# Kernel optimization log

Hardware: AMD Instinct MI355X
Metric: run time of the kernel (lower is better)

## Reference

```python
import jax, jax.numpy as jnp
import numpy as np
from jax import lax

EPS = 1e-5
NUM_HEADS = 8


def _safe_norm(x):
    # sqrt(max(sum x^2, EPS^2)) == max(||x||, EPS); grad-safe at 0
    return jnp.sqrt(jnp.maximum(jnp.sum(x * x, axis=-1, keepdims=True), EPS * EPS))


def _project(x):
    norm = _safe_norm(x)
    max_norm = 1.0 - EPS
    scale = jnp.where(norm >= max_norm, max_norm / (norm + EPS), jnp.ones_like(norm))
    return x * scale


def _logmap0(y):
    # logarithmic_map(0, y): lambda_0 = 2/(1+EPS)
    y = _project(y)
    n = _safe_norm(y)  # clamp(min=EPS) is built in
    lam = 2.0 / (1.0 + EPS)
    return (2.0 / lam) * jnp.arctanh(n) * (y / n)


def _expmap0(v):
    # exponential_map(0, v): lambda_0 = 2/(1+EPS)
    n = _safe_norm(v)
    lam = 2.0 / (1.0 + EPS)
    return _project(jnp.tanh(lam * n / 2.0) * (v / n))


def _mobius_add(x, y):
    x = _project(x)
    y = _project(y)
    xy = jnp.sum(x * y, axis=-1, keepdims=True)
    xn = jnp.sum(x * x, axis=-1, keepdims=True)
    yn = jnp.sum(y * y, axis=-1, keepdims=True)
    num = (1.0 + 2.0 * xy + yn) * x + (1.0 - xn) * y
    den = 1.0 + 2.0 * xy + xn * yn + EPS
    return _project(num / den)


def _hyp_linear(x, W, b):
    # HyperbolicLinear.forward: project -> logmap0 -> linear -> expmap0 -> mobius-add bias
    x = _project(x)
    xt = _logmap0(x)
    t = xt @ W.T
    r = _expmap0(t)
    r = _mobius_add(r, jnp.broadcast_to(b, r.shape))
    return r


def setup_inputs() -> dict:
    key = jax.random.key(0)
    ks = jax.random.split(key, 11)
    B, S, E = 4, 512, 512

    def xavier(k, shape):
        bound = np.sqrt(6.0 / (shape[0] + shape[1]))
        return jax.random.uniform(k, shape, jnp.float32, -bound, bound)

    return {
        "query": jax.random.normal(ks[0], (B, S, E), jnp.float32),
        "key": jax.random.normal(ks[1], (B, S, E), jnp.float32),
        "value": jax.random.normal(ks[2], (B, S, E), jnp.float32),
        "Wq": xavier(ks[3], (E, E)), "bq": 0.01 * jax.random.normal(ks[4], (E,), jnp.float32),
        "Wk": xavier(ks[5], (E, E)), "bk": 0.01 * jax.random.normal(ks[6], (E,), jnp.float32),
        "Wv": xavier(ks[7], (E, E)), "bv": 0.01 * jax.random.normal(ks[8], (E,), jnp.float32),
        "Wo": xavier(ks[9], (E, E)), "bo": 0.01 * jax.random.normal(ks[10], (E,), jnp.float32),
    }


def reference(query, key, value, Wq, bq, Wk, bk, Wv, bv, Wo, bo):
    B, S, E = query.shape
    H = NUM_HEADS
    D = E // H

    Q = _hyp_linear(query, Wq, bq).reshape(B, S, H, D).transpose(0, 2, 1, 3)  # [B,H,S,D]
    K = _hyp_linear(key, Wk, bk).reshape(B, S, H, D).transpose(0, 2, 1, 3)
    V = _hyp_linear(value, Wv, bv).reshape(B, S, H, D).transpose(0, 2, 1, 3)

    # Pairwise Poincare distance: d(q,k) = acosh(1 + 2||q-k||^2/((1-|q|^2)(1-|k|^2)) + EPS)
    q = _project(Q)
    k = _project(K)
    qn = jnp.sum(q * q, axis=-1)  # [B,H,S]
    kn = jnp.sum(k * k, axis=-1)  # [B,H,S]
    qk = jnp.einsum('bhqd,bhkd->bhqk', q, k)
    num = jnp.maximum(qn[..., :, None] + kn[..., None, :] - 2.0 * qk, 0.0)
    den = jnp.maximum((1.0 - qn)[..., :, None] * (1.0 - kn)[..., None, :], EPS)
    dist = jnp.arccosh(1.0 + 2.0 * num / den + EPS)  # [B,H,Sq,Sk]
    attn = jax.nn.softmax(-dist, axis=-1)

    # Sequential Mobius-add accumulation over key/value positions
    wt = jnp.moveaxis(attn, 3, 0)  # [Sk,B,H,Sq]
    vt = jnp.moveaxis(V, 2, 0)     # [Sk,B,H,D]

    @jax.checkpoint
    def step(ws, wv):
        wj, vj = wv  # wj: [B,H,Sq], vj: [B,H,D]
        return _mobius_add(ws, wj[..., None] * vj[:, :, None, :]), None

    ws0 = jnp.zeros((B, H, S, D), query.dtype)
    attended, _ = lax.scan(step, ws0, (wt, vt))  # [B,H,Sq,D]

    attended = attended.transpose(0, 2, 1, 3).reshape(B, S, E)
    return _hyp_linear(attended, Wo, bo)
```

## Files before the change

kernel.cpp:

```cpp
#include <hip/hip_runtime.h>
#include <math.h>

#define EPS  1e-5f
#define EPS2 1e-10f
#define MAXN (1.0f - EPS)

using short8  = __attribute__((ext_vector_type(8))) short;
using floatx4 = __attribute__((ext_vector_type(4))) float;
using float2v = __attribute__((ext_vector_type(2))) float;

template <int CTRL>
static __device__ __forceinline__ float qperm(float x) {
  return __int_as_float(__builtin_amdgcn_update_dpp(
      __float_as_int(x), __float_as_int(x), CTRL, 0xF, 0xF, false));
}
#define QP_XOR1    0xB1
#define QP_XOR2    0x4E
#define QP_HALFMIR 0x141

#if __has_builtin(__builtin_elementwise_fma)
static __device__ __forceinline__ float2v fma2(float2v a, float2v b, float2v c) {
  return __builtin_elementwise_fma(a, b, c);
}
#else
static __device__ __forceinline__ float2v fma2(float2v a, float2v b, float2v c) {
  float2v r; r.x = fmaf(a.x, b.x, c.x); r.y = fmaf(a.y, b.y, c.y); return r;
}
#endif

static __device__ __forceinline__ int pack_hi2(float a, float b) {
  return (int)((__float_as_uint(a) >> 16) | (__float_as_uint(b) & 0xFFFF0000u));
}
static __device__ __forceinline__ float hi_of(float a) {
  return __uint_as_float(__float_as_uint(a) & 0xFFFF0000u);
}

static __device__ __forceinline__ float logmap_f(float ss) {
  const float r = sqrtf(fmaxf(ss, EPS2));
  float at;
  if (r >= MAXN) {
    at = 0.5f * logf((r * (2.0f - EPS) + EPS) / (EPS * (1.0f + r)));
  } else {
    at = 0.5f * logf((1.0f + r) / (1.0f - r));
  }
  return (1.0f + EPS) * at / r;
}

__global__ __launch_bounds__(256) void k_splitW(
    const float* __restrict__ W0, const float* __restrict__ W1, const float* __restrict__ W2,
    int* __restrict__ h0, int* __restrict__ l0,
    int* __restrict__ h1, int* __restrict__ l1,
    int* __restrict__ h2, int* __restrict__ l2) {
  const int row = blockIdx.x, z = blockIdx.y, t = threadIdx.x;
  const float* W = (z == 0) ? W0 : ((z == 1) ? W1 : W2);
  int* H = (z == 0) ? h0 : ((z == 1) ? h1 : h2);
  int* L = (z == 0) ? l0 : ((z == 1) ? l1 : l2);
  const float2 w = *(const float2*)&W[(size_t)row * 512 + 2 * t];
  H[(size_t)row * 256 + t] = pack_hi2(w.x, w.y);
  L[(size_t)row * 256 + t] = pack_hi2(w.x - hi_of(w.x), w.y - hi_of(w.y));
}

__global__ __launch_bounds__(256) void k_gemm_mfma(
    const float* __restrict__ A0, const float* __restrict__ A1, const float* __restrict__ A2,
    const int* __restrict__ Wh0, const int* __restrict__ Wl0,
    const int* __restrict__ Wh1, const int* __restrict__ Wl1,
    const int* __restrict__ Wh2, const int* __restrict__ Wl2,
    float* __restrict__ Cbase) {
  const int z = blockIdx.z;
  const float* A = (z == 0) ? A0 : ((z == 1) ? A1 : A2);
  const int* Wh = (z == 0) ? Wh0 : ((z == 1) ? Wh1 : Wh2);
  const int* Wl = (z == 0) ? Wl0 : ((z == 1) ? Wl1 : Wl2);
  float* C = Cbase + (size_t)z * (2048 * 512);
  __shared__ int Ahi[64][36], Alo[64][36], Whi[64][36], Wlo[64][36];
  __shared__ float f_lds[64];
  const int t = threadIdx.x;
  const int n0 = blockIdx.x * 64;
  const int m0 = blockIdx.y * 64;
  const int row = t >> 2, c0 = (t & 3) * 16, ci = (t & 3) * 8;
  const int w = t >> 6, lane = t & 63;
  const int quad = lane >> 4, l16 = lane & 15;
  const int mw = (w & 1) * 32, nw = (w >> 1) * 32;
  floatx4 acc[2][2];
#pragma unroll
  for (int i = 0; i < 2; ++i)
#pragma unroll
    for (int j = 0; j < 2; ++j) acc[i][j] = (floatx4){0.f, 0.f, 0.f, 0.f};
  float ssq = 0.0f;

  for (int k0 = 0; k0 < 512; k0 += 64) {
    float4 av[4];
#pragma unroll
    for (int i = 0; i < 4; ++i)
      av[i] = *(const float4*)&A[(size_t)(n0 + row) * 512 + k0 + c0 + 4 * i];
    const size_t wbase = (size_t)(m0 + row) * 256 + (k0 >> 1) + ci;
    const int4 wh0 = *(const int4*)&Wh[wbase];
    const int4 wh1 = *(const int4*)&Wh[wbase + 4];
    const int4 wl0 = *(const int4*)&Wl[wbase];
    const int4 wl1 = *(const int4*)&Wl[wbase + 4];
    int pAh[8], pAl[8];
#pragma unroll
    for (int i = 0; i < 4; ++i) {
      ssq = fmaf(av[i].x, av[i].x, ssq); ssq = fmaf(av[i].y, av[i].y, ssq);
      ssq = fmaf(av[i].z, av[i].z, ssq); ssq = fmaf(av[i].w, av[i].w, ssq);
      pAh[2 * i]     = pack_hi2(av[i].x, av[i].y);
      pAh[2 * i + 1] = pack_hi2(av[i].z, av[i].w);
      pAl[2 * i]     = pack_hi2(av[i].x - hi_of(av[i].x), av[i].y - hi_of(av[i].y));
      pAl[2 * i + 1] = pack_hi2(av[i].z - hi_of(av[i].z), av[i].w - hi_of(av[i].w));
    }
    __syncthreads();
    *(int4*)&Ahi[row][ci]     = *(int4*)&pAh[0];
    *(int4*)&Ahi[row][ci + 4] = *(int4*)&pAh[4];
    *(int4*)&Alo[row][ci]     = *(int4*)&pAl[0];
    *(int4*)&Alo[row][ci + 4] = *(int4*)&pAl[4];
    *(int4*)&Whi[row][ci]     = wh0;
    *(int4*)&Whi[row][ci + 4] = wh1;
    *(int4*)&Wlo[row][ci]     = wl0;
    *(int4*)&Wlo[row][ci + 4] = wl1;
    __syncthreads();
#pragma unroll
    for (int kk = 0; kk < 64; kk += 32) {
      short8 ah[2], al[2], bh[2], bl[2];
#pragma unroll
      for (int i = 0; i < 2; ++i) {
        ah[i] = *(const short8*)&((const short*)Ahi[mw + i * 16 + l16])[kk + quad * 8];
        al[i] = *(const short8*)&((const short*)Alo[mw + i * 16 + l16])[kk + quad * 8];
        bh[i] = *(const short8*)&((const short*)Whi[nw + i * 16 + l16])[kk + quad * 8];
        bl[i] = *(const short8*)&((const short*)Wlo[nw + i * 16 + l16])[kk + quad * 8];
      }
#pragma unroll
      for (int i = 0; i < 2; ++i)
#pragma unroll
        for (int j = 0; j < 2; ++j) {
          acc[i][j] = __builtin_amdgcn_mfma_f32_16x16x32_bf16(ah[i], bh[j], acc[i][j], 0, 0, 0);
          acc[i][j] = __builtin_amdgcn_mfma_f32_16x16x32_bf16(ah[i], bl[j], acc[i][j], 0, 0, 0);
          acc[i][j] = __builtin_amdgcn_mfma_f32_16x16x32_bf16(al[i], bh[j], acc[i][j], 0, 0, 0);
        }
    }
  }
  ssq += qperm<QP_XOR1>(ssq);
  ssq += qperm<QP_XOR2>(ssq);
  if ((t & 3) == 0) f_lds[row] = logmap_f(ssq);
  __syncthreads();
#pragma unroll
  for (int i = 0; i < 2; ++i) {
    const int lrow_base = mw + i * 16 + quad * 4;
#pragma unroll
    for (int r = 0; r < 4; ++r) {
      const float fv = f_lds[lrow_base + r];
#pragma unroll
      for (int j = 0; j < 2; ++j)
        C[(size_t)(n0 + lrow_base + r) * 512 + m0 + nw + j * 16 + l16] = fv * acc[i][j][r];
    }
  }
}

__global__ __launch_bounds__(256) void k_post(const float* __restrict__ tin,
                                              const float* __restrict__ b0,
                                              const float* __restrict__ b1,
                                              const float* __restrict__ b2,
                                              float* __restrict__ o0, float* __restrict__ o1,
                                              float* __restrict__ o2,
                                              float* __restrict__ nrm0, float* __restrict__ nrm1,
                                              float* __restrict__ nrm2,
                                              float* __restrict__ rowsum_init,
                                              int* __restrict__ qhi, int* __restrict__ qlo,
                                              int* __restrict__ khi, int* __restrict__ klo,
                                              int final_mode) {
  const int nrow = blockIdx.x, z = blockIdx.y, t = threadIdx.x;
  const float* tv = tin + ((size_t)z * 2048 + nrow) * 512;
  const float* bias = (z == 0) ? b0 : ((z == 1) ? b1 : b2);
  const int e0 = 2 * t;
  const float2 tp = *(const float2*)&tv[e0];
  const float2 bp = *(const float2*)&bias[e0];
  float p_tt = tp.x * tp.x + tp.y * tp.y;
  float p_tb = tp.x * bp.x + tp.y * bp.y;
  float p_bb = bp.x * bp.x + bp.y * bp.y;
#pragma unroll
  for (int m = 32; m; m >>= 1) {
    p_tt += __shfl_xor(p_tt, m, 64);
    p_tb += __shfl_xor(p_tb, m, 64);
    p_bb += __shfl_xor(p_bb, m, 64);
  }
  __shared__ float red[4][3];
  const int lane = t & 63, w = t >> 6;
  if (lane == 0) { red[w][0] = p_tt; red[w][1] = p_tb; red[w][2] = p_bb; }
  __syncthreads();
  const float s_tt = red[0][0] + red[1][0] + red[2][0] + red[3][0];
  const float s_tb = red[0][1] + red[1][1] + red[2][1] + red[3][1];
  const float s_bb = red[0][2] + red[1][2] + red[2][2] + red[3][2];
  const float tn = sqrtf(fmaxf(s_tt, EPS2));
  const float th = tanhf(tn / (1.0f + EPS));
  const float g = th / tn;
  const float rnorm = th * (sqrtf(s_tt) / tn);
  const float sr = (rnorm >= MAXN) ? (MAXN / (rnorm + EPS)) : 1.0f;
  const float gr = g * sr;
  const float rn = (rnorm * sr) * (rnorm * sr);
  const float bnorm = sqrtf(fmaxf(s_bb, EPS2));
  const float sb = (bnorm >= MAXN) ? (MAXN / (bnorm + EPS)) : 1.0f;
  const float xy = gr * sb * s_tb;
  const float yn = (sb * sb) * s_bb;
  const float Af = 1.0f + 2.0f * xy + yn;
  const float Cf = 1.0f - rn;
  const float den = 1.0f + 2.0f * xy + rn * yn + EPS;
  const float id = 1.0f / den;
  const float on_raw = (Af * Af * rn + 2.0f * Af * Cf * xy + Cf * Cf * yn) * (id * id);
  const float no = sqrtf(fmaxf(on_raw, EPS2));
  const float so = (no >= MAXN) ? (MAXN / (no + EPS)) : 1.0f;
  const float ms = id * so;
  const float ca = gr * Af * ms;
  const float cb = sb * Cf * ms;
  const float v0 = ca * tp.x + cb * bp.x;
  const float v1 = ca * tp.y + cb * bp.y;
  if (final_mode) {
    float2 o; o.x = v0; o.y = v1;
    *(float2*)&o0[(size_t)nrow * 512 + e0] = o;
    return;
  }
  float hp = v0 * v0 + v1 * v1;
#pragma unroll
  for (int m = 16; m; m >>= 1) hp += __shfl_xor(hp, m, 64);
  const float hnr = sqrtf(fmaxf(hp, EPS2));
  float sh = 1.0f;
  if (z != 2) sh = (hnr >= MAXN) ? (MAXN / (hnr + EPS)) : 1.0f;
  float* nz = (z == 0) ? nrm0 : ((z == 1) ? nrm1 : nrm2);
  const int b = nrow >> 9, s = nrow & 511, h = e0 >> 6, d = e0 & 63;
  const float ox = v0 * sh, oy = v1 * sh;
  if (z == 2) {
    float2 o; o.x = ox; o.y = oy;
    *(float2*)&o2[(((size_t)(b * 8 + h) * 512 + s) * 64 + d)] = o;
  } else {
    int* Hp = (z == 0) ? qhi : khi;
    int* Lp = (z == 0) ? qlo : klo;
    const size_t pidx = ((size_t)(b * 8 + h) * 512 + s) * 32 + (d >> 1);
    Hp[pidx] = pack_hi2(ox, oy);
    Lp[pidx] = pack_hi2(ox - hi_of(ox), oy - hi_of(oy));
  }
  if ((t & 31) == 0) nz[(size_t)(b * 8 + h) * 512 + s] = hp * sh * sh;
  if (z == 0 && t < 8) rowsum_init[((size_t)(nrow >> 9) * 8 + t) * 512 + (nrow & 511)] = 0.0f;
}

__global__ __launch_bounds__(256) void k_logits(const int* __restrict__ QhiG,
                                                const int* __restrict__ QloG,
                                                const int* __restrict__ KhiG,
                                                const int* __restrict__ KloG,
                                                const float* __restrict__ qn,
                                                const float* __restrict__ kn,
                                                float* __restrict__ attn,
                                                float* __restrict__ rowsum) {
  const int bh = blockIdx.z;
  const int i0 = blockIdx.x * 64;
  const int jh = blockIdx.y;
  __shared__ int Qhi[64][36], Qlo[64][36], Khi[64][36], Klo[64][36];
  const int t = threadIdx.x;
  const int row = t >> 2, ci = (t & 3) * 8;
  const int w = t >> 6, lane = t & 63;
  const int quad = lane >> 4, l16 = lane & 15;
  const int mw = (w & 1) * 32, nw = (w >> 1) * 32;
  {
    const size_t qbase = ((size_t)bh * 512 + i0 + row) * 32 + ci;
    *(int4*)&Qhi[row][ci]     = *(const int4*)&QhiG[qbase];
    *(int4*)&Qhi[row][ci + 4] = *(const int4*)&QhiG[qbase + 4];
    *(int4*)&Qlo[row][ci]     = *(const int4*)&QloG[qbase];
    *(int4*)&Qlo[row][ci + 4] = *(const int4*)&QloG[qbase + 4];
  }
  float qni_r[2][4], rq_r[2][4];
#pragma unroll
  for (int i = 0; i < 2; ++i)
#pragma unroll
    for (int r = 0; r < 4; ++r) {
      const int grow = i0 + mw + i * 16 + quad * 4 + r;
      qni_r[i][r] = qn[(size_t)bh * 512 + grow];
      rq_r[i][r]  = 1.0f - qni_r[i][r];
    }
  float rs_acc[2][4];
#pragma unroll
  for (int i = 0; i < 2; ++i)
#pragma unroll
    for (int r = 0; r < 4; ++r) rs_acc[i][r] = 0.0f;

  for (int j0i = 0; j0i < 4; ++j0i) {
    const int j0 = jh * 256 + j0i * 64;
    const size_t kbase = ((size_t)bh * 512 + j0 + row) * 32 + ci;
    const int4 kh0 = *(const int4*)&KhiG[kbase];
    const int4 kh1 = *(const int4*)&KhiG[kbase + 4];
    const int4 kl0 = *(const int4*)&KloG[kbase];
    const int4 kl1 = *(const int4*)&KloG[kbase + 4];
    __syncthreads();
    *(int4*)&Khi[row][ci]     = kh0;
    *(int4*)&Khi[row][ci + 4] = kh1;
    *(int4*)&Klo[row][ci]     = kl0;
    *(int4*)&Klo[row][ci + 4] = kl1;
    __syncthreads();
    floatx4 acc[2][2];
#pragma unroll
    for (int i = 0; i < 2; ++i)
#pragma unroll
      for (int j = 0; j < 2; ++j) acc[i][j] = (floatx4){0.f, 0.f, 0.f, 0.f};
#pragma unroll
    for (int kk = 0; kk < 64; kk += 32) {
      short8 ah[2], al[2], bhv[2], blv[2];
#pragma unroll
      for (int i = 0; i < 2; ++i) {
        ah[i]  = *(const short8*)&((const short*)Qhi[mw + i * 16 + l16])[kk + quad * 8];
        al[i]  = *(const short8*)&((const short*)Qlo[mw + i * 16 + l16])[kk + quad * 8];
        bhv[i] = *(const short8*)&((const short*)Khi[nw + i * 16 + l16])[kk + quad * 8];
        blv[i] = *(const short8*)&((const short*)Klo[nw + i * 16 + l16])[kk + quad * 8];
      }
#pragma unroll
      for (int i = 0; i < 2; ++i)
#pragma unroll
        for (int j = 0; j < 2; ++j) {
          acc[i][j] = __builtin_amdgcn_mfma_f32_16x16x32_bf16(ah[i], bhv[j], acc[i][j], 0, 0, 0);
          acc[i][j] = __builtin_amdgcn_mfma_f32_16x16x32_bf16(ah[i], blv[j], acc[i][j], 0, 0, 0);
          acc[i][j] = __builtin_amdgcn_mfma_f32_16x16x32_bf16(al[i], bhv[j], acc[i][j], 0, 0, 0);
        }
    }
#pragma unroll
    for (int i = 0; i < 2; ++i)
#pragma unroll
      for (int r = 0; r < 4; ++r) {
        const int grow = i0 + mw + i * 16 + quad * 4 + r;
        const float qni = qni_r[i][r];
        const float rq  = rq_r[i][r];
#pragma unroll
        for (int j = 0; j < 2; ++j) {
          const int gcol = j0 + nw + j * 16 + l16;
          const float knj = kn[(size_t)bh * 512 + gcol];
          const float num = fmaxf(qni + knj - 2.0f * acc[i][j][r], 0.0f);
          const float den = fmaxf(rq * (1.0f - knj), EPS);
          const float wv = fmaf(2.0f * num, __builtin_amdgcn_rcpf(den), EPS);
          const float s_ = 1.0f + wv + sqrtf(wv * (wv + 2.0f));
          const float rr = __builtin_amdgcn_rcpf(s_);
          rs_acc[i][r] += rr;
          attn[((size_t)bh * 512 + grow) * 512 + gcol] = rr;
        }
      }
  }
#pragma unroll
  for (int i = 0; i < 2; ++i)
#pragma unroll
    for (int r = 0; r < 4; ++r) {
      float v = rs_acc[i][r];
      v += __shfl_xor(v, 1, 64); v += __shfl_xor(v, 2, 64);
      v += __shfl_xor(v, 4, 64); v += __shfl_xor(v, 8, 64);
      if (l16 == 0)
        atomicAdd(&rowsum[(size_t)bh * 512 + i0 + mw + i * 16 + quad * 4 + r], v);
    }
}

__global__ __launch_bounds__(256) void k_scan(const float* __restrict__ V,
                                              const float* __restrict__ vn,
                                              const float* __restrict__ rw,
                                              const float* __restrict__ rowsum,
                                              float* __restrict__ att) {
  __shared__ __align__(16) float v_lds[64 * 64];
  __shared__ __align__(16) float swyn_lds[64 * 66];
  const int blk = blockIdx.x;
  const int bh = blk >> 4;
  const int i0 = (blk & 15) * 32;
  const int t = threadIdx.x;
  const int lane = t & 63, w = t >> 6;
  const int row_blk = w * 8 + (lane >> 3);
  const int sub = lane & 7;
  const int d0 = sub * 8;
  const float* Vb = V + (size_t)bh * 512 * 64;
  const float* vnb = vn + (size_t)bh * 512;
  const float* arow = rw + ((size_t)bh * 512 + i0 + row_blk) * 512;
  const float inv_s = __builtin_amdgcn_rcpf(rowsum[(size_t)bh * 512 + i0 + row_blk]);

  float2v wsv[4];
#pragma unroll
  for (int k = 0; k < 4; ++k) wsv[k] = (float2v){0.f, 0.f};
  float xn = 0.0f;

  for (int jc = 0; jc < 512; jc += 64) {
#pragma unroll
    for (int it = 0; it < 4; ++it) {
      const int idx4 = it * 256 + t;
      *(float4*)&v_lds[idx4 * 4] = *(const float4*)&Vb[(size_t)jc * 64 + idx4 * 4];
    }
    const float4 a0 = *(const float4*)&arow[jc + sub * 8];
    const float4 a1 = *(const float4*)&arow[jc + sub * 8 + 4];
    const float4 n0 = *(const float4*)&vnb[jc + sub * 8];
    const float4 n1 = *(const float4*)&vnb[jc + sub * 8 + 4];
    const float wq[8] = {a0.x, a0.y, a0.z, a0.w, a1.x, a1.y, a1.z, a1.w};
    const float nq[8] = {n0.x, n0.y, n0.z, n0.w, n1.x, n1.y, n1.z, n1.w};
#pragma unroll
    for (int e = 0; e < 8; ++e) {
      const float wgt = wq[e] * inv_s;
      float2 p; p.x = wgt; p.y = (wgt * wgt) * nq[e];
      *(float2*)&swyn_lds[(sub * 8 + e) * 66 + row_blk * 2] = p;
    }
    __syncthreads();

    float4 pv0 = *(const float4*)&v_lds[d0];
    float4 pv1 = *(const float4*)&v_lds[d0 + 4];
    float2 psy = *(const float2*)&swyn_lds[row_blk * 2];
#pragma unroll
    for (int j = 0; j < 64; ++j) {
      const float4 v0 = pv0;
      const float4 v1 = pv1;
      const float2 sy2 = psy;
      if (j < 63) {
        pv0 = *(const float4*)&v_lds[(j + 1) * 64 + d0];
        pv1 = *(const float4*)&v_lds[(j + 1) * 64 + d0 + 4];
        psy = *(const float2*)&swyn_lds[(j + 1) * 66 + row_blk * 2];
      }
      const float2v vv0 = {v0.x, v0.y}, vv1 = {v0.z, v0.w};
      const float2v vv2 = {v1.x, v1.y}, vv3 = {v1.z, v1.w};
      const float sw = sy2.x, yn = sy2.y;
      const float xnyn1 = fmaf(xn, yn, 1.0f + EPS);
      const float sxy   = xn + yn;
      const float ynp1  = 1.0f + yn;
      const float Cfsw  = (1.0f - xn) * sw;
      float2v da = wsv[0] * vv0;
      da = fma2(wsv[1], vv1, da);
      float2v db = wsv[2] * vv2;
      db = fma2(wsv[3], vv3, db);
      const float2v sv = da + db;
      float d = sv.x + sv.y;
      d += qperm<QP_XOR1>(d);
      d += qperm<QP_XOR2>(d);
      d += qperm<QP_HALFMIR>(d);
      const float xy  = sw * d;
      const float den = fmaf(2.0f, xy, xnyn1);
      const float s2  = fmaf(2.0f, xy, sxy);
      const float Af  = fmaf(2.0f, xy, ynp1);
      const float id  = __builtin_amdgcn_rcpf(den);
      const float dn  = den - EPS;
      const float am  = Af * id;
      const float cm  = Cfsw * id;
      xn = (s2 * id) * (dn * id);
      const float2v amv = {am, am};
      const float2v cmv = {cm, cm};
      wsv[0] = fma2(amv, wsv[0], cmv * vv0);
      wsv[1] = fma2(amv, wsv[1], cmv * vv1);
      wsv[2] = fma2(amv, wsv[2], cmv * vv2);
      wsv[3] = fma2(amv, wsv[3], cmv * vv3);
    }
    __syncthreads();
  }
  const int b = bh >> 3, h = bh & 7;
  float* o = att + (((size_t)b * 512 + i0 + row_blk) * 512 + h * 64 + d0);
  float4 s0; s0.x = wsv[0].x; s0.y = wsv[0].y; s0.z = wsv[1].x; s0.w = wsv[1].y;
  float4 s1; s1.x = wsv[2].x; s1.y = wsv[2].y; s1.z = wsv[3].x; s1.w = wsv[3].y;
  *(float4*)&o[0] = s0;
  *(float4*)&o[4] = s1;
}

extern "C" void kernel_launch(void* const* d_in, const int* in_sizes, int n_in,
                              void* d_out, int out_size, void* d_ws, size_t ws_size,
                              hipStream_t stream) {
  const float* query = (const float*)d_in[0];
  const float* key_  = (const float*)d_in[1];
  const float* value = (const float*)d_in[2];
  const float* Wq = (const float*)d_in[3];
  const float* bq = (const float*)d_in[4];
  const float* Wk = (const float*)d_in[5];
  const float* bk = (const float*)d_in[6];
  const float* Wv = (const float*)d_in[7];
  const float* bv = (const float*)d_in[8];
  const float* Wo = (const float*)d_in[9];
  const float* bo = (const float*)d_in[10];
  float* ws = (float*)d_ws;
  const size_t M = 1u << 20;
  int* qhi = (int*)ws;
  int* qlo = (int*)ws + 524288;
  int* khi = (int*)ws + 1048576;
  int* klo = (int*)ws + 1572864;
  float* Vb     = ws + 2 * M;
  float* qn     = ws + 3 * M;
  float* kn     = qn + 16384;
  float* vn     = kn + 16384;
  float* rowsum = vn + 16384;
  int* wsl = (int*)(ws + 3 * M + 65536);
  int* whq = wsl,          * wlq = wsl + 131072;
  int* whk = wsl + 262144, * wlk = wsl + 393216;
  int* whv = wsl + 524288, * wlv = wsl + 655360;
  float* rw     = ws + 4 * M;
  float* t3     = ws + 12 * M;
  int* who  = (int*)(ws + 12 * M);
  int* wlo_ = (int*)(ws + 12 * M) + 131072;
  float* att    = ws + 15 * M;
  float* to_    = ws + 16 * M;

  k_splitW<<<dim3(512, 3), 256, 0, stream>>>(Wq, Wk, Wv, whq, wlq, whk, wlk, whv, wlv);
  k_gemm_mfma<<<dim3(32, 8, 3), 256, 0, stream>>>(query, key_, value,
                                                  whq, wlq, whk, wlk, whv, wlv, t3);
  k_post<<<dim3(2048, 3), 256, 0, stream>>>(t3, bq, bk, bv, nullptr, nullptr, Vb,
                                            qn, kn, vn, rowsum, qhi, qlo, khi, klo, 0);
  k_splitW<<<dim3(512, 1), 256, 0, stream>>>(Wo, Wo, Wo, who, wlo_, who, wlo_, who, wlo_);
  k_logits<<<dim3(8, 2, 32), 256, 0, stream>>>(qhi, qlo, khi, klo, qn, kn, rw, rowsum);
  k_scan<<<512, 256, 0, stream>>>(Vb, vn, rw, rowsum, att);
  k_gemm_mfma<<<dim3(32, 8, 1), 256, 0, stream>>>(att, att, att,
                                                  who, wlo_, who, wlo_, who, wlo_, to_);
  k_post<<<dim3(2048, 1), 256, 0, stream>>>(to_, bo, bo, bo, (float*)d_out,
                                            nullptr, nullptr, nullptr, nullptr, nullptr,
                                            nullptr, nullptr, nullptr, nullptr, nullptr, 1);
}
```

Measured before the change: 230.8 us.

## Recompute attention weights inside scan kernel instead of storing full attention matrix

The logits kernel now only accumulates row sums and no longer writes the 32 MB attention matrix. The scan kernel recomputes each 32x64 tile of Poincare-distance weights with split-bf16 MFMA from staged Q/K fragments, normalises by the row sum, and writes them straight into LDS. This removes a large global write and re-read, in exchange for computing the logits twice and adding LDS usage and an extra barrier per chunk in the latency-bound scan loop.

```diff
diff --git a/kernel.cpp b/kernel.cpp
--- a/kernel.cpp
+++ b/kernel.cpp
@@ -245,7 +245,6 @@
                                                 const int* __restrict__ KloG,
                                                 const float* __restrict__ qn,
                                                 const float* __restrict__ kn,
-                                                float* __restrict__ attn,
                                                 float* __restrict__ rowsum) {
   const int bh = blockIdx.z;
   const int i0 = blockIdx.x * 64;
@@ -319,7 +318,6 @@
     for (int i = 0; i < 2; ++i)
 #pragma unroll
       for (int r = 0; r < 4; ++r) {
-        const int grow = i0 + mw + i * 16 + quad * 4 + r;
         const float qni = qni_r[i][r];
         const float rq  = rq_r[i][r];
 #pragma unroll
@@ -332,7 +330,6 @@
           const float s_ = 1.0f + wv + sqrtf(wv * (wv + 2.0f));
           const float rr = __builtin_amdgcn_rcpf(s_);
           rs_acc[i][r] += rr;
-          attn[((size_t)bh * 512 + grow) * 512 + gcol] = rr;
         }
       }
   }
@@ -350,11 +347,19 @@
 
 __global__ __launch_bounds__(256) void k_scan(const float* __restrict__ V,
                                               const float* __restrict__ vn,
-                                              const float* __restrict__ rw,
+                                              const float* __restrict__ kn,
+                                              const float* __restrict__ qn,
+                                              const int* __restrict__ QhiG,
+                                              const int* __restrict__ QloG,
+                                              const int* __restrict__ KhiG,
+                                              const int* __restrict__ KloG,
                                               const float* __restrict__ rowsum,
                                               float* __restrict__ att) {
   __shared__ __align__(16) float v_lds[64 * 64];
   __shared__ __align__(16) float swyn_lds[64 * 66];
+  __shared__ int Qh_l[32][36], Ql_l[32][36];
+  __shared__ int Kh_l[64][36], Kl_l[64][36];
+  __shared__ float kn_t[64], vn_t[64], qn_l[32], inv_l[32];
   const int blk = blockIdx.x;
   const int bh = blk >> 4;
   const int i0 = (blk & 15) * 32;
@@ -363,10 +368,20 @@
   const int row_blk = w * 8 + (lane >> 3);
   const int sub = lane & 7;
   const int d0 = sub * 8;
+  const int quad = lane >> 4, l16 = lane & 15;
   const float* Vb = V + (size_t)bh * 512 * 64;
   const float* vnb = vn + (size_t)bh * 512;
-  const float* arow = rw + ((size_t)bh * 512 + i0 + row_blk) * 512;
-  const float inv_s = __builtin_amdgcn_rcpf(rowsum[(size_t)bh * 512 + i0 + row_blk]);
+  const float* knb = kn + (size_t)bh * 512;
+
+  {
+    const int qr = t >> 3;
+    const int qc = (t & 7) * 4;
+    const size_t qb = ((size_t)bh * 512 + i0 + qr) * 32 + qc;
+    *(int4*)&Qh_l[qr][qc] = *(const int4*)&QhiG[qb];
+    *(int4*)&Ql_l[qr][qc] = *(const int4*)&QloG[qb];
+  }
+  if (t < 32) inv_l[t] = __builtin_amdgcn_rcpf(rowsum[(size_t)bh * 512 + i0 + t]);
+  else if (t < 64) qn_l[t - 32] = qn[(size_t)bh * 512 + i0 + (t - 32)];
 
   float2v wsv[4];
 #pragma unroll
@@ -374,22 +389,62 @@
   float xn = 0.0f;
 
   for (int jc = 0; jc < 512; jc += 64) {
+    __syncthreads();
 #pragma unroll
     for (int it = 0; it < 4; ++it) {
       const int idx4 = it * 256 + t;
       *(float4*)&v_lds[idx4 * 4] = *(const float4*)&Vb[(size_t)jc * 64 + idx4 * 4];
     }
-    const float4 a0 = *(const float4*)&arow[jc + sub * 8];
-    const float4 a1 = *(const float4*)&arow[jc + sub * 8 + 4];
-    const float4 n0 = *(const float4*)&vnb[jc + sub * 8];
-    const float4 n1 = *(const float4*)&vnb[jc + sub * 8 + 4];
-    const float wq[8] = {a0.x, a0.y, a0.z, a0.w, a1.x, a1.y, a1.z, a1.w};
-    const float nq[8] = {n0.x, n0.y, n0.z, n0.w, n1.x, n1.y, n1.z, n1.w};
-#pragma unroll
-    for (int e = 0; e < 8; ++e) {
-      const float wgt = wq[e] * inv_s;
-      float2 p; p.x = wgt; p.y = (wgt * wgt) * nq[e];
-      *(float2*)&swyn_lds[(sub * 8 + e) * 66 + row_blk * 2] = p;
+    {
+      const int kr = t >> 2;
+      const int kc = (t & 3) * 8;
+      const size_t kb = ((size_t)bh * 512 + jc + kr) * 32 + kc;
+      *(int4*)&Kh_l[kr][kc]     = *(const int4*)&KhiG[kb];
+      *(int4*)&Kh_l[kr][kc + 4] = *(const int4*)&KhiG[kb + 4];
+      *(int4*)&Kl_l[kr][kc]     = *(const int4*)&KloG[kb];
+      *(int4*)&Kl_l[kr][kc + 4] = *(const int4*)&KloG[kb + 4];
+    }
+    if (t < 16)      *(float4*)&kn_t[t * 4] = *(const float4*)&knb[jc + t * 4];
+    else if (t < 32) *(float4*)&vn_t[(t - 16) * 4] = *(const float4*)&vnb[jc + (t - 16) * 4];
+    __syncthreads();
+
+    {
+      const int nw2 = w * 16;
+      floatx4 qacc[2];
+      qacc[0] = (floatx4){0.f, 0.f, 0.f, 0.f};
+      qacc[1] = (floatx4){0.f, 0.f, 0.f, 0.f};
+#pragma unroll
+      for (int kk = 0; kk < 64; kk += 32) {
+        const short8 bh_ = *(const short8*)&((const short*)Kh_l[nw2 + l16])[kk + quad * 8];
+        const short8 bl_ = *(const short8*)&((const short*)Kl_l[nw2 + l16])[kk + quad * 8];
+#pragma unroll
+        for (int i = 0; i < 2; ++i) {
+          const short8 ah_ = *(const short8*)&((const short*)Qh_l[i * 16 + l16])[kk + quad * 8];
+          const short8 al_ = *(const short8*)&((const short*)Ql_l[i * 16 + l16])[kk + quad * 8];
+          qacc[i] = __builtin_amdgcn_mfma_f32_16x16x32_bf16(ah_, bh_, qacc[i], 0, 0, 0);
+          qacc[i] = __builtin_amdgcn_mfma_f32_16x16x32_bf16(ah_, bl_, qacc[i], 0, 0, 0);
+          qacc[i] = __builtin_amdgcn_mfma_f32_16x16x32_bf16(al_, bh_, qacc[i], 0, 0, 0);
+        }
+      }
+      const int col = nw2 + l16;
+      const float knj = kn_t[col];
+      const float vnj = vn_t[col];
+#pragma unroll
+      for (int i = 0; i < 2; ++i)
+#pragma unroll
+        for (int r = 0; r < 4; ++r) {
+          const int qrow = i * 16 + quad * 4 + r;
+          const float qni = qn_l[qrow];
+          const float rq  = 1.0f - qni;
+          const float num = fmaxf(qni + knj - 2.0f * qacc[i][r], 0.0f);
+          const float den = fmaxf(rq * (1.0f - knj), EPS);
+          const float wv = fmaf(2.0f * num, __builtin_amdgcn_rcpf(den), EPS);
+          const float s_ = 1.0f + wv + sqrtf(wv * (wv + 2.0f));
+          const float rr = __builtin_amdgcn_rcpf(s_);
+          const float sw = rr * inv_l[qrow];
+          float2 p; p.x = sw; p.y = (sw * sw) * vnj;
+          *(float2*)&swyn_lds[col * 66 + qrow * 2] = p;
+        }
     }
     __syncthreads();
 
@@ -438,7 +493,6 @@
       wsv[2] = fma2(amv, wsv[2], cmv * vv2);
       wsv[3] = fma2(amv, wsv[3], cmv * vv3);
     }
-    __syncthreads();
   }
   const int b = bh >> 3, h = bh & 7;
   float* o = att + (((size_t)b * 512 + i0 + row_blk) * 512 + h * 64 + d0);
@@ -477,7 +531,6 @@
   int* whq = wsl,          * wlq = wsl + 131072;
   int* whk = wsl + 262144, * wlk = wsl + 393216;
   int* whv = wsl + 524288, * wlv = wsl + 655360;
-  float* rw     = ws + 4 * M;
   float* t3     = ws + 12 * M;
   int* who  = (int*)(ws + 12 * M);
   int* wlo_ = (int*)(ws + 12 * M) + 131072;
@@ -490,8 +543,8 @@
   k_post<<<dim3(2048, 3), 256, 0, stream>>>(t3, bq, bk, bv, nullptr, nullptr, Vb,
                                             qn, kn, vn, rowsum, qhi, qlo, khi, klo, 0);
   k_splitW<<<dim3(512, 1), 256, 0, stream>>>(Wo, Wo, Wo, who, wlo_, who, wlo_, who, wlo_);
-  k_logits<<<dim3(8, 2, 32), 256, 0, stream>>>(qhi, qlo, khi, klo, qn, kn, rw, rowsum);
-  k_scan<<<512, 256, 0, stream>>>(Vb, vn, rw, rowsum, att);
+  k_logits<<<dim3(8, 2, 32), 256, 0, stream>>>(qhi, qlo, khi, klo, qn, kn, rowsum);
+  k_scan<<<512, 256, 0, stream>>>(Vb, vn, kn, qn, qhi, qlo, khi, klo, rowsum, att);
   k_gemm_mfma<<<dim3(32, 8, 1), 256, 0, stream>>>(att, att, att,
                                                   who, wlo_, who, wlo_, who, wlo_, to_);
   k_post<<<dim3(2048, 1), 256, 0, stream>>>(to_, bo, bo, bo, (float*)d_out,
```

After: 240.6 us. 4.2% more time.
